# Performance work log

Hardware: AMD Instinct MI355X
Metric: run time of the kernel (lower is better)

## Reference

```python
import jax, jax.numpy as jnp
import numpy as np

N_NODES = 100000
N_EDGES = 1600000
D_IN = 128
D_HID = 128


def setup_inputs() -> dict:
    key = jax.random.key(0)
    ks = jax.random.split(key, 8)
    x = jax.random.normal(ks[0], (N_NODES, D_IN), dtype=jnp.float32)
    edge_index = jax.random.randint(ks[1], (2, N_EDGES), 0, N_NODES, dtype=jnp.int64)
    s = 1.0 / np.sqrt(D_IN)
    W_root1 = jax.random.normal(ks[2], (D_IN, D_HID), dtype=jnp.float32) * s
    W_rel1 = jax.random.normal(ks[3], (D_IN, D_HID), dtype=jnp.float32) * s
    b1 = jnp.zeros((D_HID,), dtype=jnp.float32)
    sh = 1.0 / np.sqrt(D_HID)
    W_root2 = jax.random.normal(ks[4], (D_HID, D_HID), dtype=jnp.float32) * sh
    W_rel2 = jax.random.normal(ks[5], (D_HID, D_HID), dtype=jnp.float32) * sh
    b2 = jnp.zeros((D_HID,), dtype=jnp.float32)
    return {"x": x, "edge_index": edge_index, "W_root1": W_root1, "W_rel1": W_rel1,
            "b1": b1, "W_root2": W_root2, "W_rel2": W_rel2, "b2": b2}


def graph_conv(x, src, dst, W_root, W_rel, b):
    # PyG GraphConv: out_i = x_i @ W_root + (sum_{j in N(i)} x_j) @ W_rel + b
    agg = jax.ops.segment_sum(x[src], dst, num_segments=N_NODES)  # [N, d]
    return x @ W_root + agg @ W_rel + b


def reference(x, edge_index, W_root1, W_rel1, b1, W_root2, W_rel2, b2):
    src, dst = edge_index[0], edge_index[1]
    h = jax.nn.relu(graph_conv(x, src, dst, W_root1, W_rel1, b1))
    # dropout is identity in eval mode (reference baseline)
    h = jax.nn.relu(graph_conv(h, src, dst, W_root2, W_rel2, b2))
    return h
```

## Files before the change

kernel.cpp:

```cpp
#include <hip/hip_runtime.h>

#define D 128
#define KTOT 256
#define GM 128
#define LPAD 8
#define LSTR (KTOT + LPAD)

#define EB1   8192
#define BKT_W 64
#define WIN   1024
#define EMAX  8192
#define HB1MAX 2048

typedef __attribute__((ext_vector_type(8))) short bf16x8;
typedef __attribute__((ext_vector_type(4))) float f32x4;

__device__ __forceinline__ unsigned short f2b(float f) {
    unsigned int u = __float_as_uint(f);
    u += 0x7fffu + ((u >> 16) & 1u);
    return (unsigned short)(u >> 16);
}
__device__ __forceinline__ float blo(unsigned int u) { return __uint_as_float(u << 16); }
__device__ __forceinline__ float bhi(unsigned int u) { return __uint_as_float(u & 0xffff0000u); }

__global__ __launch_bounds__(256) void pack_count_kernel(
    const void* __restrict__ ei, unsigned int* __restrict__ pk,
    unsigned short* __restrict__ bkt, int n_edges, int nb1,
    int* __restrict__ C)
{
    __shared__ int h[HB1MAX];
    for (int i = threadIdx.x; i < nb1; i += 256) h[i] = 0;

    const unsigned int* eiu = (const unsigned int*)ei;
    const int l = threadIdx.x & 63;
    unsigned int w0 = eiu[2 * l + 1];
    unsigned int w1 = eiu[2 * (l + 64) + 1];
    const int is64 = __all((w0 | w1) == 0u);
    __syncthreads();

    const int e0 = blockIdx.x * EB1;
    const int e1 = min(e0 + EB1, n_edges);
    for (int e = e0 + threadIdx.x; e < e1; e += 256) {
        int s, d;
        if (is64) {
            const long long* p = (const long long*)ei;
            s = (int)p[e]; d = (int)p[n_edges + e];
        } else {
            const int* p = (const int*)ei;
            s = p[e]; d = p[n_edges + e];
        }
        pk[e]  = ((unsigned int)s << 6) | (unsigned int)(d & (BKT_W - 1));
        int b = d >> 6;
        bkt[e] = (unsigned short)b;
        atomicAdd(&h[b], 1);
    }
    __syncthreads();
    int* out = C + (long long)blockIdx.x * nb1;
    for (int i = threadIdx.x; i < nb1; i += 256) out[i] = h[i];
}

__global__ __launch_bounds__(1024) void scanA_kernel(
    const int* __restrict__ C, int* __restrict__ Cs,
    int* __restrict__ blockSums, int L, int nb1, int nblk1)
{
    __shared__ int sm[1024];
    const int tid = threadIdx.x;
    const int i = blockIdx.x * 1024 + tid;
    int v = 0;
    if (i < L) {
        int b = i / nblk1, k = i - b * nblk1;
        v = C[(long long)k * nb1 + b];
    }
    int val = v;
    sm[tid] = val;
    __syncthreads();
    for (int off = 1; off < 1024; off <<= 1) {
        int t = (tid >= off) ? sm[tid - off] : 0;
        __syncthreads();
        val += t;
        sm[tid] = val;
        __syncthreads();
    }
    if (i < L) Cs[i] = val - v;
    if (tid == 1023) blockSums[blockIdx.x] = val;
}

__global__ __launch_bounds__(1024) void scan3_kernel(
    int* __restrict__ arr, const int* __restrict__ blockSums, int n)
{
    __shared__ int sm[1024];
    const int tid = threadIdx.x;
    sm[tid] = (tid < blockIdx.x) ? blockSums[tid] : 0;
    __syncthreads();
    #pragma unroll
    for (int off = 512; off > 0; off >>= 1) {
        if (tid < off) sm[tid] += sm[tid + off];
        __syncthreads();
    }
    const int i = blockIdx.x * 1024 + tid;
    if (i < n) arr[i] += sm[0];
}

__global__ __launch_bounds__(256) void s1_scatter_kernel(
    const unsigned short* __restrict__ bkt, const unsigned int* __restrict__ pk,
    const int* __restrict__ Cs, unsigned int* __restrict__ sorted,
    int n_edges, int nb1, int nblk1)
{
    __shared__ int cur[WIN];
    const int win = blockIdx.x / nblk1;
    const int blk = blockIdx.x - win * nblk1;
    const int lo  = win * WIN;
    const int hi  = min(lo + WIN, nb1);
    for (int t = threadIdx.x; t < hi - lo; t += 256)
        cur[t] = Cs[(long long)(lo + t) * nblk1 + blk];
    __syncthreads();
    const int e0 = blk * EB1;
    const int e1 = min(e0 + EB1, n_edges);
    for (int e = e0 + threadIdx.x; e < e1; e += 256) {
        int b = bkt[e];
        if (b >= lo && b < hi) {
            int pos = atomicAdd(&cur[b - lo], 1);
            sorted[pos] = pk[e];
        }
    }
}

__global__ __launch_bounds__(256) void sort_prep_kernel(
    unsigned int* __restrict__ sorted, const int* __restrict__ Cs,
    int n_edges, int n_nodes, int nb1, int nblk1, int* __restrict__ row_end,
    const float* __restrict__ x, unsigned short* __restrict__ Xb,
    long long nelem, int nbcvt,
    const float* __restrict__ Wr1, const float* __restrict__ Wl1,
    unsigned short* __restrict__ Wt1,
    const float* __restrict__ Wr2, const float* __restrict__ Wl2,
    unsigned short* __restrict__ Wt2)
{
    __shared__ unsigned int lpk[EMAX];
    __shared__ int h64[BKT_W], excl[BKT_W + 1], cur[BKT_W];
    const int bid = blockIdx.x;
    const int t = threadIdx.x;

    if (bid < nb1) {
        const int b = bid;
        const int base = Cs[(long long)b * nblk1];
        const int nextb = (b + 1 < nb1) ? Cs[(long long)(b + 1) * nblk1] : n_edges;
        const int cnt = min(nextb - base, EMAX);

        if (t < BKT_W) h64[t] = 0;
        for (int i = t; i < cnt; i += 256) lpk[i] = sorted[base + i];
        __syncthreads();
        for (int i = t; i < cnt; i += 256) atomicAdd(&h64[lpk[i] & (BKT_W - 1)], 1);
        __syncthreads();
        if (t == 0) {
            int run = 0;
            #pragma unroll
            for (int i = 0; i < BKT_W; ++i) { excl[i] = run; run += h64[i]; }
            excl[BKT_W] = run;
        }
        __syncthreads();
        const int node0 = b * BKT_W;
        const int bins = min(BKT_W, n_nodes - node0);
        if (t < bins) row_end[node0 + t] = base + excl[t + 1];
        if (t < BKT_W) cur[t] = excl[t];
        __syncthreads();
        for (int i = t; i < cnt; i += 256) {
            unsigned int p = lpk[i];
            int pos = atomicAdd(&cur[p & (BKT_W - 1)], 1);
            sorted[base + pos] = p >> 6;
        }
    } else if (bid < nb1 + nbcvt) {
        const long long i = ((long long)(bid - nb1) * 256 + t) * 8;
        if (i >= nelem) return;
        float4 a = *(const float4*)(x + i);
        float4 c2 = *(const float4*)(x + i + 4);
        bf16x8 v;
        v[0] = (short)f2b(a.x);  v[1] = (short)f2b(a.y);
        v[2] = (short)f2b(a.z);  v[3] = (short)f2b(a.w);
        v[4] = (short)f2b(c2.x); v[5] = (short)f2b(c2.y);
        v[6] = (short)f2b(c2.z); v[7] = (short)f2b(c2.w);
        *(bf16x8*)(Xb + i) = v;
    } else {
        const int cb = bid - nb1 - nbcvt;
        const float* Wr = (cb < 128) ? Wr1 : Wr2;
        const float* Wl = (cb < 128) ? Wl1 : Wl2;
        unsigned short* Wt = (cb < 128) ? Wt1 : Wt2;
        const int c = cb & 127;
        const int k = t;
        float v = (k < 128) ? Wr[k * D + c] : Wl[(k - 128) * D + c];
        Wt[c * KTOT + k] = f2b(v);
    }
}

#define ACC8(u) { a0 += blo(u.x); a1 += bhi(u.x); a2 += blo(u.y); a3 += bhi(u.y); \
                  a4 += blo(u.z); a5 += bhi(u.z); a6 += blo(u.w); a7 += bhi(u.w); }

__global__ __launch_bounds__(256) void agg_kernel(
    const unsigned short* __restrict__ src, const int* __restrict__ sorted_src,
    const int* __restrict__ row_end, unsigned short* __restrict__ dst, int n)
{
    const int node = blockIdx.x * 4 + (threadIdx.x >> 6);
    if (node >= n) return;
    const int lane = threadIdx.x & 63;
    const int j = lane >> 4;
    const int c = (lane & 15) * 8;
    const int beg = node ? row_end[node - 1] : 0;
    const int end = row_end[node];

    float a0 = 0.f, a1 = 0.f, a2 = 0.f, a3 = 0.f,
          a4 = 0.f, a5 = 0.f, a6 = 0.f, a7 = 0.f;

    int i = beg + j;
    for (; i + 12 < end; i += 16) {
        int s0 = sorted_src[i];
        int s1 = sorted_src[i + 4];
        int s2 = sorted_src[i + 8];
        int s3 = sorted_src[i + 12];
        uint4 u0 = *(const uint4*)(src + (long long)s0 * D + c);
        uint4 u1 = *(const uint4*)(src + (long long)s1 * D + c);
        uint4 u2 = *(const uint4*)(src + (long long)s2 * D + c);
        uint4 u3 = *(const uint4*)(src + (long long)s3 * D + c);
        ACC8(u0); ACC8(u1); ACC8(u2); ACC8(u3);
    }
    for (; i < end; i += 4) {
        int s0 = sorted_src[i];
        uint4 u0 = *(const uint4*)(src + (long long)s0 * D + c);
        ACC8(u0);
    }

    a0 += __shfl_xor(a0, 16); a1 += __shfl_xor(a1, 16);
    a2 += __shfl_xor(a2, 16); a3 += __shfl_xor(a3, 16);
    a4 += __shfl_xor(a4, 16); a5 += __shfl_xor(a5, 16);
    a6 += __shfl_xor(a6, 16); a7 += __shfl_xor(a7, 16);
    a0 += __shfl_xor(a0, 32); a1 += __shfl_xor(a1, 32);
    a2 += __shfl_xor(a2, 32); a3 += __shfl_xor(a3, 32);
    a4 += __shfl_xor(a4, 32); a5 += __shfl_xor(a5, 32);
    a6 += __shfl_xor(a6, 32); a7 += __shfl_xor(a7, 32);

    if (j == 0) {
        uint4 p;
        p.x = (unsigned int)f2b(a0) | ((unsigned int)f2b(a1) << 16);
        p.y = (unsigned int)f2b(a2) | ((unsigned int)f2b(a3) << 16);
        p.z = (unsigned int)f2b(a4) | ((unsigned int)f2b(a5) << 16);
        p.w = (unsigned int)f2b(a6) | ((unsigned int)f2b(a7) << 16);
        *(uint4*)(dst + (long long)node * D + c) = p;
    }
}

template <int OUT_BF16>
__global__ __launch_bounds__(512) void gemm_kernel(
    const unsigned short* __restrict__ Xop, const unsigned short* __restrict__ Aop,
    const unsigned short* __restrict__ Wt, const float* __restrict__ bias,
    void* outp, int n)
{
    __shared__ short sW[D][LSTR];
    const int tid = threadIdx.x;
    const int r0 = blockIdx.x * GM;

    for (int i = 0; i < 8; ++i) {
        int idx = tid + i * 512;
        int r = idx >> 5, c8 = idx & 31;
        bf16x8 w = *(const bf16x8*)(Wt + r * KTOT + c8 * 8);
        *(bf16x8*)&sW[r][c8 * 8] = w;
    }
    __syncthreads();

    const int w    = tid >> 6;
    const int lane = tid & 63;
    const int lr   = lane & 15;
    const int lk   = (lane >> 4) * 8;
    const int row  = r0 + w * 16 + lr;
    const bool rok = (row < n);

    f32x4 acc[8];
    #pragma unroll
    for (int ct = 0; ct < 8; ++ct) acc[ct] = (f32x4){0.f, 0.f, 0.f, 0.f};

    #pragma unroll
    for (int ks = 0; ks < 8; ++ks) {
        bf16x8 a = {};
        if (rok) {
            const unsigned short* base = (ks < 4) ? Xop : Aop;
            a = *(const bf16x8*)(base + (long long)row * D + (ks & 3) * 32 + lk);
        }
        #pragma unroll
        for (int ct = 0; ct < 8; ++ct) {
            bf16x8 bf = *(const bf16x8*)&sW[ct * 16 + lr][ks * 32 + lk];
            acc[ct] = __builtin_amdgcn_mfma_f32_16x16x32_bf16(a, bf, acc[ct], 0, 0, 0);
        }
    }

    const int rbase = r0 + w * 16 + (lane >> 4) * 4;
    #pragma unroll
    for (int ct = 0; ct < 8; ++ct) {
        const int col = ct * 16 + lr;
        const float bv = bias[col];
        #pragma unroll
        for (int j = 0; j < 4; ++j) {
            int orow = rbase + j;
            if (orow < n) {
                float val = fmaxf(acc[ct][j] + bv, 0.f);
                if (OUT_BF16) {
                    ((unsigned short*)outp)[(long long)orow * D + col] = f2b(val);
                } else {
                    ((float*)outp)[(long long)orow * D + col] = val;
                }
            }
        }
    }
}

static inline size_t align_up(size_t v, size_t a) { return (v + a - 1) & ~(a - 1); }

extern "C" void kernel_launch(void* const* d_in, const int* in_sizes, int n_in,
                              void* d_out, int out_size, void* d_ws, size_t ws_size,
                              hipStream_t stream) {
    const float* x   = (const float*)d_in[0];
    const void*  ei  = d_in[1];
    const float* Wr1 = (const float*)d_in[2];
    const float* Wl1 = (const float*)d_in[3];
    const float* b1  = (const float*)d_in[4];
    const float* Wr2 = (const float*)d_in[5];
    const float* Wl2 = (const float*)d_in[6];
    const float* b2  = (const float*)d_in[7];
    float* out = (float*)d_out;

    const int n_nodes = in_sizes[0] / D;
    const int n_edges = in_sizes[1] / 2;

    const int nb1   = (n_nodes + BKT_W - 1) / BKT_W;
    const int nblk1 = (n_edges + EB1 - 1) / EB1;
    const int L     = nb1 * nblk1;
    const int npass = (nb1 + WIN - 1) / WIN;
    const int nbL   = (L + 1023) / 1024;

    char* ws = (char*)d_ws;
    size_t off_rs   = 0;
    size_t off_bs   = align_up(off_rs + 4 * (size_t)(n_nodes + 1), 256);
    size_t off_ssrc = align_up(off_bs + 4 * 1024, 256);
    size_t off_wt1  = align_up(off_ssrc + 4 * (size_t)n_edges, 256);
    size_t off_wt2  = align_up(off_wt1 + 2 * (size_t)D * KTOT, 256);
    size_t off_xb   = align_up(off_wt2 + 2 * (size_t)D * KTOT, 256);
    size_t off_ab   = align_up(off_xb + 2 * (size_t)n_nodes * D, 256);

    int* row_end         = (int*)(ws + off_rs);
    int* blockSums       = (int*)(ws + off_bs);
    unsigned int* sorted = (unsigned int*)(ws + off_ssrc);
    unsigned short* Wt1  = (unsigned short*)(ws + off_wt1);
    unsigned short* Wt2  = (unsigned short*)(ws + off_wt2);
    unsigned short* Xb   = (unsigned short*)(ws + off_xb);
    unsigned short* Ab   = (unsigned short*)(ws + off_ab);
    unsigned int*   pk  = (unsigned int*)(ws + off_xb);
    unsigned short* bkt = (unsigned short*)(pk + n_edges);
    int* C  = (int*)(ws + off_ab);
    int* Cs = C + L;

    const int gemm_blocks = (n_nodes + GM - 1) / GM;
    const int agg_blocks  = (n_nodes + 3) / 4;
    const long long nfeat = (long long)n_nodes * D;
    const int nbcvt = (int)((nfeat / 8 + 255) / 256);

    pack_count_kernel<<<nblk1, 256, 0, stream>>>(ei, pk, bkt, n_edges, nb1, C);
    scanA_kernel<<<nbL, 1024, 0, stream>>>(C, Cs, blockSums, L, nb1, nblk1);
    scan3_kernel<<<nbL, 1024, 0, stream>>>(Cs, blockSums, L);
    s1_scatter_kernel<<<nblk1 * npass, 256, 0, stream>>>(
        bkt, pk, Cs, sorted, n_edges, nb1, nblk1);

    sort_prep_kernel<<<nb1 + nbcvt + 256, 256, 0, stream>>>(
        sorted, Cs, n_edges, n_nodes, nb1, nblk1, row_end,
        x, Xb, nfeat, nbcvt, Wr1, Wl1, Wt1, Wr2, Wl2, Wt2);

    agg_kernel<<<agg_blocks, 256, 0, stream>>>(
        Xb, (const int*)sorted, row_end, Ab, n_nodes);
    gemm_kernel<1><<<gemm_blocks, 512, 0, stream>>>(Xb, Ab, Wt1, b1, Ab, n_nodes);

    agg_kernel<<<agg_blocks, 256, 0, stream>>>(
        Ab, (const int*)sorted, row_end, Xb, n_nodes);
    gemm_kernel<0><<<gemm_blocks, 512, 0, stream>>>(Ab, Xb, Wt2, b2, out, n_nodes);
}
```

Before: 237.7 us.

## Fuse neighbor aggregation into GEMM kernel, keeping aggregates in registers

Replaces the separate aggregation and GEMM kernels with one fused kernel per layer. Each lane of the 16-row MFMA tile gathers its node's neighbor rows directly, accumulates in fp32 registers, converts to bf16, and feeds the result as the second half of the K dimension. This removes the intermediate aggregate write and read and two kernel launches. In exchange, parallelism over edges drops: each lane now handles a whole node's neighbors serially, with only 4 lanes per row and 64 B row segments, so gathers are less coalesced, load imbalance grows with degree variance, and register pressure rises.

Measured after the change: 265.9 us. 11.9% more time.

```diff
diff --git a/kernel.cpp b/kernel.cpp
--- a/kernel.cpp
+++ b/kernel.cpp
@@ -191,66 +191,16 @@
     }
 }
 
-#define ACC8(u) { a0 += blo(u.x); a1 += bhi(u.x); a2 += blo(u.y); a3 += bhi(u.y); \
-                  a4 += blo(u.z); a5 += bhi(u.z); a6 += blo(u.w); a7 += bhi(u.w); }
-
-__global__ __launch_bounds__(256) void agg_kernel(
-    const unsigned short* __restrict__ src, const int* __restrict__ sorted_src,
-    const int* __restrict__ row_end, unsigned short* __restrict__ dst, int n)
-{
-    const int node = blockIdx.x * 4 + (threadIdx.x >> 6);
-    if (node >= n) return;
-    const int lane = threadIdx.x & 63;
-    const int j = lane >> 4;
-    const int c = (lane & 15) * 8;
-    const int beg = node ? row_end[node - 1] : 0;
-    const int end = row_end[node];
-
-    float a0 = 0.f, a1 = 0.f, a2 = 0.f, a3 = 0.f,
-          a4 = 0.f, a5 = 0.f, a6 = 0.f, a7 = 0.f;
-
-    int i = beg + j;
-    for (; i + 12 < end; i += 16) {
-        int s0 = sorted_src[i];
-        int s1 = sorted_src[i + 4];
-        int s2 = sorted_src[i + 8];
-        int s3 = sorted_src[i + 12];
-        uint4 u0 = *(const uint4*)(src + (long long)s0 * D + c);
-        uint4 u1 = *(const uint4*)(src + (long long)s1 * D + c);
-        uint4 u2 = *(const uint4*)(src + (long long)s2 * D + c);
-        uint4 u3 = *(const uint4*)(src + (long long)s3 * D + c);
-        ACC8(u0); ACC8(u1); ACC8(u2); ACC8(u3);
-    }
-    for (; i < end; i += 4) {
-        int s0 = sorted_src[i];
-        uint4 u0 = *(const uint4*)(src + (long long)s0 * D + c);
-        ACC8(u0);
-    }
-
-    a0 += __shfl_xor(a0, 16); a1 += __shfl_xor(a1, 16);
-    a2 += __shfl_xor(a2, 16); a3 += __shfl_xor(a3, 16);
-    a4 += __shfl_xor(a4, 16); a5 += __shfl_xor(a5, 16);
-    a6 += __shfl_xor(a6, 16); a7 += __shfl_xor(a7, 16);
-    a0 += __shfl_xor(a0, 32); a1 += __shfl_xor(a1, 32);
-    a2 += __shfl_xor(a2, 32); a3 += __shfl_xor(a3, 32);
-    a4 += __shfl_xor(a4, 32); a5 += __shfl_xor(a5, 32);
-    a6 += __shfl_xor(a6, 32); a7 += __shfl_xor(a7, 32);
-
-    if (j == 0) {
-        uint4 p;
-        p.x = (unsigned int)f2b(a0) | ((unsigned int)f2b(a1) << 16);
-        p.y = (unsigned int)f2b(a2) | ((unsigned int)f2b(a3) << 16);
-        p.z = (unsigned int)f2b(a4) | ((unsigned int)f2b(a5) << 16);
-        p.w = (unsigned int)f2b(a6) | ((unsigned int)f2b(a7) << 16);
-        *(uint4*)(dst + (long long)node * D + c) = p;
-    }
-}
+#define ACCQ(t, u) { agf[t][0] += blo(u.x); agf[t][1] += bhi(u.x); \
+                     agf[t][2] += blo(u.y); agf[t][3] += bhi(u.y); \
+                     agf[t][4] += blo(u.z); agf[t][5] += bhi(u.z); \
+                     agf[t][6] += blo(u.w); agf[t][7] += bhi(u.w); }
 
 template <int OUT_BF16>
-__global__ __launch_bounds__(512) void gemm_kernel(
-    const unsigned short* __restrict__ Xop, const unsigned short* __restrict__ Aop,
-    const unsigned short* __restrict__ Wt, const float* __restrict__ bias,
-    void* outp, int n)
+__global__ __launch_bounds__(512, 4) void fused_layer_kernel(
+    const unsigned short* __restrict__ Xop, const int* __restrict__ sorted_src,
+    const int* __restrict__ row_end, const unsigned short* __restrict__ Wt,
+    const float* __restrict__ bias, void* outp, int n)
 {
     __shared__ short sW[D][LSTR];
     const int tid = threadIdx.x;
@@ -262,29 +212,78 @@
         bf16x8 w = *(const bf16x8*)(Wt + r * KTOT + c8 * 8);
         *(bf16x8*)&sW[r][c8 * 8] = w;
     }
-    __syncthreads();
 
     const int w    = tid >> 6;
     const int lane = tid & 63;
     const int lr   = lane & 15;
-    const int lk   = (lane >> 4) * 8;
+    const int q8   = (lane >> 4) * 8;
     const int row  = r0 + w * 16 + lr;
     const bool rok = (row < n);
 
+    float agf[4][8];
+    #pragma unroll
+    for (int t = 0; t < 4; ++t)
+        #pragma unroll
+        for (int j = 0; j < 8; ++j) agf[t][j] = 0.f;
+
+    int beg = 0, end = 0;
+    if (rok) {
+        beg = row ? row_end[row - 1] : 0;
+        end = row_end[row];
+    }
+    int i = beg;
+    for (; i + 1 < end; i += 2) {
+        int s0 = sorted_src[i];
+        int s1 = sorted_src[i + 1];
+        const unsigned short* rb0 = Xop + (size_t)s0 * D + q8;
+        const unsigned short* rb1 = Xop + (size_t)s1 * D + q8;
+        uint4 u0 = *(const uint4*)(rb0);
+        uint4 u1 = *(const uint4*)(rb0 + 32);
+        uint4 u2 = *(const uint4*)(rb0 + 64);
+        uint4 u3 = *(const uint4*)(rb0 + 96);
+        uint4 v0 = *(const uint4*)(rb1);
+        uint4 v1 = *(const uint4*)(rb1 + 32);
+        uint4 v2 = *(const uint4*)(rb1 + 64);
+        uint4 v3 = *(const uint4*)(rb1 + 96);
+        ACCQ(0, u0); ACCQ(1, u1); ACCQ(2, u2); ACCQ(3, u3);
+        ACCQ(0, v0); ACCQ(1, v1); ACCQ(2, v2); ACCQ(3, v3);
+    }
+    if (i < end) {
+        int s0 = sorted_src[i];
+        const unsigned short* rb0 = Xop + (size_t)s0 * D + q8;
+        uint4 u0 = *(const uint4*)(rb0);
+        uint4 u1 = *(const uint4*)(rb0 + 32);
+        uint4 u2 = *(const uint4*)(rb0 + 64);
+        uint4 u3 = *(const uint4*)(rb0 + 96);
+        ACCQ(0, u0); ACCQ(1, u1); ACCQ(2, u2); ACCQ(3, u3);
+    }
+
+    bf16x8 afr[4];
+    #pragma unroll
+    for (int t = 0; t < 4; ++t) {
+        #pragma unroll
+        for (int j = 0; j < 8; ++j) afr[t][j] = (short)f2b(agf[t][j]);
+    }
+
+    __syncthreads();
+
     f32x4 acc[8];
     #pragma unroll
     for (int ct = 0; ct < 8; ++ct) acc[ct] = (f32x4){0.f, 0.f, 0.f, 0.f};
 
     #pragma unroll
     for (int ks = 0; ks < 8; ++ks) {
-        bf16x8 a = {};
-        if (rok) {
-            const unsigned short* base = (ks < 4) ? Xop : Aop;
-            a = *(const bf16x8*)(base + (long long)row * D + (ks & 3) * 32 + lk);
+        bf16x8 a;
+        if (ks < 4) {
+            a = (bf16x8){};
+            if (rok)
+                a = *(const bf16x8*)(Xop + (size_t)row * D + ks * 32 + q8);
+        } else {
+            a = afr[ks - 4];
         }
         #pragma unroll
         for (int ct = 0; ct < 8; ++ct) {
-            bf16x8 bf = *(const bf16x8*)&sW[ct * 16 + lr][ks * 32 + lk];
+            bf16x8 bf = *(const bf16x8*)&sW[ct * 16 + lr][ks * 32 + q8];
             acc[ct] = __builtin_amdgcn_mfma_f32_16x16x32_bf16(a, bf, acc[ct], 0, 0, 0);
         }
     }
@@ -300,9 +299,9 @@
             if (orow < n) {
                 float val = fmaxf(acc[ct][j] + bv, 0.f);
                 if (OUT_BF16) {
-                    ((unsigned short*)outp)[(long long)orow * D + col] = f2b(val);
+                    ((unsigned short*)outp)[(size_t)orow * D + col] = f2b(val);
                 } else {
-                    ((float*)outp)[(long long)orow * D + col] = val;
+                    ((float*)outp)[(size_t)orow * D + col] = val;
                 }
             }
         }
@@ -355,7 +354,6 @@
     int* Cs = C + L;
 
     const int gemm_blocks = (n_nodes + GM - 1) / GM;
-    const int agg_blocks  = (n_nodes + 3) / 4;
     const long long nfeat = (long long)n_nodes * D;
     const int nbcvt = (int)((nfeat / 8 + 255) / 256);
 
@@ -369,11 +367,9 @@
         sorted, Cs, n_edges, n_nodes, nb1, nblk1, row_end,
         x, Xb, nfeat, nbcvt, Wr1, Wl1, Wt1, Wr2, Wl2, Wt2);
 
-    agg_kernel<<<agg_blocks, 256, 0, stream>>>(
-        Xb, (const int*)sorted, row_end, Ab, n_nodes);
-    gemm_kernel<1><<<gemm_blocks, 512, 0, stream>>>(Xb, Ab, Wt1, b1, Ab, n_nodes);
-
-    agg_kernel<<<agg_blocks, 256, 0, stream>>>(
-        Ab, (const int*)sorted, row_end, Xb, n_nodes);
-    gemm_kernel<0><<<gemm_blocks, 512, 0, stream>>>(Ab, Xb, Wt2, b2, out, n_nodes);
-}
+    fused_layer_kernel<1><<<gemm_blocks, 512, 0, stream>>>(
+        Xb, (const int*)sorted, row_end, Wt1, b1, Ab, n_nodes);
+
+    fused_layer_kernel<0><<<gemm_blocks, 512, 0, stream>>>(
+        Ab, (const int*)sorted, row_end, Wt2, b2, out, n_nodes);
+}
```
